# Optimization experiments

Hardware: AMD Instinct MI355X
Metric: run time of the kernel (lower is better)

The kernel has to match this reference:

```python
import jax, jax.numpy as jnp
import numpy as np

EPS = 1e-5
HEADS = 16
HEAD_DIM = 64
SIG_SCALE = HEAD_DIM ** (-0.25)
DEFAULT_BIAS = -3.0

def layernorm(x, scale, offset):
    mu = jnp.mean(x, axis=-1, keepdims=True)
    var = jnp.mean(jnp.square(x - mu), axis=-1, keepdims=True)
    return (x - mu) * jax.lax.rsqrt(var + EPS) * scale + offset

def setup_inputs() -> dict:
    key = jax.random.key(0)
    ks = jax.random.split(key, 16)
    B, Nq, Nk, D, A = 2, 2048, 2048, 1024, 1024
    s = 0.02
    return {
        "query_feats": jax.random.normal(ks[0], (B, Nq, D), jnp.float32),
        "key_feats": jax.random.normal(ks[1], (B, Nk, D), jnp.float32),
        "Wq": jax.random.normal(ks[2], (A, D), jnp.float32) * s,
        "Wk": jax.random.normal(ks[3], (A, D), jnp.float32) * s,
        "Wv": jax.random.normal(ks[4], (A, D), jnp.float32) * s,
        "Wo": jax.random.normal(ks[5], (D, A), jnp.float32) * s,
        "qn_scale": jnp.ones((HEAD_DIM,), jnp.float32),
        "qn_bias": jnp.zeros((HEAD_DIM,), jnp.float32),
        "kn_scale": jnp.ones((HEAD_DIM,), jnp.float32),
        "kn_bias": jnp.zeros((HEAD_DIM,), jnp.float32),
        "ln_q_scale": jnp.ones((D,), jnp.float32),
        "ln_q_bias": jnp.zeros((D,), jnp.float32),
        "ln_out_scale": jnp.ones((D,), jnp.float32),
        "ln_out_bias": jnp.zeros((D,), jnp.float32),
        "gamma": jnp.full((D,), 1e-5, jnp.float32),
    }

def reference(query_feats, key_feats, Wq, Wk, Wv, Wo, qn_scale, qn_bias, kn_scale, kn_bias, ln_q_scale, ln_q_bias, ln_out_scale, ln_out_bias, gamma):
    B, Nq, _ = query_feats.shape
    Nk = key_feats.shape[1]
    residual = query_feats
    xq = layernorm(query_feats, ln_q_scale, ln_q_bias)  # norm_first
    # projections (torch Linear: x @ W.T)
    q = (xq @ Wq.T).reshape(B, Nq, HEADS, HEAD_DIM).transpose(0, 2, 1, 3)
    k = (key_feats @ Wk.T).reshape(B, Nk, HEADS, HEAD_DIM).transpose(0, 2, 1, 3)
    v = (key_feats @ Wv.T).reshape(B, Nk, HEADS, HEAD_DIM).transpose(0, 2, 1, 3)
    # qk-norm over head_dim, then fixed sigmoid scale
    q = layernorm(q, qn_scale, qn_bias) * SIG_SCALE
    k = layernorm(k, kn_scale, kn_bias) * SIG_SCALE
    scores = jnp.einsum('bhqd,bhkd->bhqk', q, k) + DEFAULT_BIAS
    # hardware-optimized sigmoid: 0.5*(1+tanh(0.5*x))
    attn = 0.5 * (1.0 + jnp.tanh(0.5 * scores))
    ctx = jnp.einsum('bhqk,bhkd->bhqd', attn, v)
    ctx = ctx.transpose(0, 2, 1, 3).reshape(B, Nq, HEADS * HEAD_DIM)
    out = ctx @ Wo.T
    out = gamma * out
    out = residual + out
    out = layernorm(out, ln_out_scale, ln_out_bias)  # post_norm
    return out
```

## Files before the change

kernel.cpp:

```cpp
#include <hip/hip_runtime.h>

typedef unsigned short u16;
typedef unsigned int u32;
typedef __bf16 bf16x8 __attribute__((ext_vector_type(8)));
typedef float f32x4 __attribute__((ext_vector_type(4)));
typedef float f32x16 __attribute__((ext_vector_type(16)));
typedef u16 u16x8 __attribute__((ext_vector_type(8)));
typedef u16 u16x4 __attribute__((ext_vector_type(4)));
typedef u32 u32x2 __attribute__((ext_vector_type(2)));
typedef u32 u32x4 __attribute__((ext_vector_type(4)));

#define LN_EPS 1e-5f
#define SIG_SCALE_F 0.35355339059327379f
#define NLOG2E -1.4426950408889634f
#define BIAS_L2E 4.328085122666891f

__device__ __forceinline__ u16 f2bf(float f) {
    u32 u = __builtin_bit_cast(u32, f);
    u32 r = u + 0x7fffu + ((u >> 16) & 1u);
    return (u16)(r >> 16);
}
__device__ __forceinline__ float bf2f(u16 v) {
    return __builtin_bit_cast(float, (u32)v << 16);
}
__device__ __forceinline__ u32 pk_hi(float a, float b) {
    return __builtin_amdgcn_perm(__builtin_bit_cast(u32, b), __builtin_bit_cast(u32, a),
                                 0x07060302u);
}
__device__ __forceinline__ float fast_rcp(float x) {
    float r = __builtin_bit_cast(float, 0x7EF311C3u - __builtin_bit_cast(u32, x));
    r = r * __builtin_fmaf(-x, r, 2.0f);
    r = r * __builtin_fmaf(-x, r, 2.0f);
    return r;
}

__device__ __forceinline__ void gload16(const u16* g, u16* lds) {
    __builtin_amdgcn_global_load_lds(
        (const __attribute__((address_space(1))) u32*)g,
        (__attribute__((address_space(3))) u32*)lds, 16, 0, 0);
}

__device__ __forceinline__ void gemm_core(f32x4 acc[4][4],
                                          const u16* __restrict__ A, const u16* __restrict__ B,
                                          int Kiter, int lda, int ldb,
                                          long m0, long n0, u16* As, u16* Bs) {
    const int tid = threadIdx.x;
    const int lane = tid & 63;
    const int wave = tid >> 6;
    const int r15 = lane & 15;
    const int qd = lane >> 4;
    const int wm = (wave >> 1) * 64;
    const int wn = (wave & 1) * 64;

    const int srow = wave * 16 + (lane >> 2);
    const int c0 = (lane & 3) ^ (srow & 3);
    const u16* Ap0 = A + (m0 + srow) * lda + c0 * 8;
    const u16* Ap1 = A + (m0 + srow + 64) * lda + c0 * 8;
    const u16* Bp0 = B + (n0 + srow) * ldb + c0 * 8;
    const u16* Bp1 = B + (n0 + srow + 64) * ldb + c0 * 8;
    u16* As0 = As + wave * 512;
    u16* As1 = As + (wave + 4) * 512;
    u16* Bs0 = Bs + wave * 512;
    u16* Bs1 = Bs + (wave + 4) * 512;

    for (int kt = 0; kt < Kiter; kt += 32) {
        __syncthreads();
        gload16(Ap0 + kt, As0);
        gload16(Ap1 + kt, As1);
        gload16(Bp0 + kt, Bs0);
        gload16(Bp1 + kt, Bs1);
        __syncthreads();
        bf16x8 af[4], bfr[4];
#pragma unroll
        for (int i = 0; i < 4; i++) {
            int row = wm + i * 16 + r15;
            af[i] = *(const bf16x8*)(As + row * 32 + ((qd ^ (row & 3)) * 8));
        }
#pragma unroll
        for (int j = 0; j < 4; j++) {
            int row = wn + j * 16 + r15;
            bfr[j] = *(const bf16x8*)(Bs + row * 32 + ((qd ^ (row & 3)) * 8));
        }
#pragma unroll
        for (int i = 0; i < 4; i++)
#pragma unroll
            for (int j = 0; j < 4; j++)
                acc[i][j] = __builtin_amdgcn_mfma_f32_16x16x32_bf16(af[i], bfr[j], acc[i][j], 0, 0, 0);
    }
}

__global__ __launch_bounds__(256, 3) void gemm_qkv(const u16* __restrict__ xq, const u16* __restrict__ keyb,
                                                   const u16* __restrict__ Wqb, const u16* __restrict__ Wkb,
                                                   const u16* __restrict__ Wvb,
                                                   const float* __restrict__ qns, const float* __restrict__ qnb,
                                                   const float* __restrict__ kns, const float* __restrict__ knb,
                                                   u16* __restrict__ qln, u16* __restrict__ kln,
                                                   u16* __restrict__ vt) {
    __shared__ __attribute__((aligned(16))) u16 As[128 * 32];
    __shared__ __attribute__((aligned(16))) u16 Bs[128 * 32];
    const int z = blockIdx.z;
    const u16* A = (z == 0) ? xq : keyb;
    const u16* B = (z == 0) ? Wqb : ((z == 1) ? Wkb : Wvb);
    const long m0 = (long)blockIdx.x * 128;
    const long n0 = (long)blockIdx.y * 128;

    f32x4 acc[4][4];
#pragma unroll
    for (int i = 0; i < 4; i++)
#pragma unroll
        for (int j = 0; j < 4; j++) acc[i][j] = (f32x4){0.f, 0.f, 0.f, 0.f};

    gemm_core(acc, A, B, 1024, 1024, 1024, m0, n0, As, Bs);

    const int lane = threadIdx.x & 63;
    const int wave = threadIdx.x >> 6;
    const int r15 = lane & 15;
    const int qd = lane >> 4;
    const int wm = (wave >> 1) * 64;
    const int wn = (wave & 1) * 64;

    if (z <= 1) {
        u16* C = (z == 0) ? qln : kln;
        const float* sc_ = (z == 0) ? qns : kns;
        const float* bs_ = (z == 0) ? qnb : knb;
        const float post = (z == 0) ? SIG_SCALE_F * NLOG2E : SIG_SCALE_F;
        float scl[4], bia[4];
#pragma unroll
        for (int j = 0; j < 4; j++) {
            scl[j] = sc_[j * 16 + r15] * post;
            bia[j] = bs_[j * 16 + r15] * post;
        }
#pragma unroll
        for (int i = 0; i < 4; i++) {
#pragma unroll
            for (int rr = 0; rr < 4; rr++) {
                float a0 = acc[i][0][rr], a1 = acc[i][1][rr], a2 = acc[i][2][rr], a3 = acc[i][3][rr];
                float s1 = (a0 + a1) + (a2 + a3);
                float s2 = __builtin_fmaf(a3, a3,
                           __builtin_fmaf(a2, a2, __builtin_fmaf(a1, a1, a0 * a0)));
#pragma unroll
                for (int off = 1; off <= 8; off <<= 1) {
                    s1 += __shfl_xor(s1, off, 64);
                    s2 += __shfl_xor(s2, off, 64);
                }
                float mu = s1 * (1.0f / 64.0f);
                float var = __builtin_fmaf(-mu, mu, s2 * (1.0f / 64.0f));
                float rs = rsqrtf(var + LN_EPS);
                long row = m0 + wm + i * 16 + qd * 4 + rr;
#pragma unroll
                for (int j = 0; j < 4; j++) {
                    long col = n0 + wn + j * 16 + r15;
                    float o = __builtin_fmaf((acc[i][j][rr] - mu) * rs, scl[j], bia[j]);
                    C[row * 1024 + col] = f2bf(o);
                }
            }
        }
    } else {
#pragma unroll
        for (int i = 0; i < 4; i++)
#pragma unroll
            for (int rr = 0; rr < 4; rr++) {
                int grow = (int)(m0 + wm + i * 16 + qd * 4 + rr);
                int bb = grow >> 11;
                int kk = grow & 2047;
#pragma unroll
                for (int j = 0; j < 4; j++) {
                    int col = (int)(n0 + wn + j * 16 + r15);
                    int hh = col >> 6;
                    int dd = col & 63;
                    vt[((size_t)(bb * 16 + hh) * 64 + dd) * 2048 + kk] = f2bf(acc[i][j][rr]);
                }
            }
    }
}

__global__ __launch_bounds__(256, 4) void gemm_o(const u16* __restrict__ ctx, const u16* __restrict__ Wob,
                                                 u16* __restrict__ opre) {
    __shared__ __attribute__((aligned(16))) u16 As[128 * 32];
    __shared__ __attribute__((aligned(16))) u16 Bs[128 * 32];
    const int z = blockIdx.z;
    const int koff = z * 512;
    u16* C = opre + (size_t)z * 4194304;
    const long m0 = (long)blockIdx.x * 128;
    const long n0 = (long)blockIdx.y * 128;
    f32x4 acc[4][4];
#pragma unroll
    for (int i = 0; i < 4; i++)
#pragma unroll
        for (int j = 0; j < 4; j++) acc[i][j] = (f32x4){0.f, 0.f, 0.f, 0.f};
    gemm_core(acc, ctx + koff, Wob + koff, 512, 1024, 1024, m0, n0, As, Bs);

    const int lane = threadIdx.x & 63;
    const int wave = threadIdx.x >> 6;
    const int r15 = lane & 15;
    const int qd = lane >> 4;
    const int wm = (wave >> 1) * 64;
    const int wn = (wave & 1) * 64;
#pragma unroll
    for (int i = 0; i < 4; i++)
#pragma unroll
        for (int rr = 0; rr < 4; rr++) {
            long row = m0 + wm + i * 16 + qd * 4 + rr;
#pragma unroll
            for (int j = 0; j < 4; j++)
                C[row * 1024 + n0 + wn + j * 16 + r15] = f2bf(acc[i][j][rr]);
        }
}

__device__ __forceinline__ bf16x8 frag64(const u16* base, int row, int kidx) {
    return *(const bf16x8*)(base + row * 64 + ((kidx ^ (row & 7)) * 8));
}

__global__ __launch_bounds__(512, 4) void attn_sigmoid_v12(const u16* __restrict__ q,
                                                           const u16* __restrict__ k,
                                                           const u16* __restrict__ vt,
                                                           u16* __restrict__ ctx) {
    __shared__ __attribute__((aligned(16))) u16 Sh[8192 + 16384 + 16384];
    u16* Qs = Sh;
    u16* Ks = Sh + 8192;
    u16* Vs = Sh + 8192 + 16384;
    float* Obuf = (float*)(Sh + 8192);

    const int tid = threadIdx.x;
    const int lane = tid & 63;
    const int wave = tid >> 6;
    const int l31 = lane & 31;
    const int h = lane >> 5;
    const int qsub = wave & 3;
    const int kh = wave >> 2;
    const int hd = blockIdx.x;
    const int q0 = blockIdx.y * 128;
    const int b = blockIdx.z;
    const int bh = b * 16 + hd;

    const int lr0 = lane >> 3;
    const int lc0 = lane & 7;
    const int wsub = wave & 3;
    const int kbeg = kh * 1024;

    auto kptr = [&](int slot) { return Ks + (slot * 2 + kh) * 4096; };
    auto vptr = [&](int slot) { return (slot == 2 ? Sh : Vs + slot * 8192) + kh * 4096; };

    auto stageKV = [&](int kslot, int vslot, int kc) {
        u16* kd = kptr(kslot);
        u16* vd = vptr(vslot);
#pragma unroll
        for (int i = 0; i < 2; i++) {
            int s = wsub * 2 + i;
            int row = s * 8 + lr0;
            int c = lc0 ^ (row & 7);
            gload16(k + (size_t)(b * 2048 + kc + row) * 1024 + hd * 64 + c * 8, kd + s * 512);
            gload16(vt + (size_t)(bh * 64 + row) * 2048 + kc + c * 8, vd + s * 512);
        }
    };

    {
#pragma unroll
        for (int i = 0; i < 2; i++) {
            int s = wave * 2 + i;
            int row = s * 8 + lr0;
            int c = lc0 ^ (row & 7);
            gload16(q + (size_t)(b * 2048 + q0 + row) * 1024 + hd * 64 + c * 8, Qs + s * 512);
        }
        stageKV(0, 0, kbeg);
    }
    __syncthreads();
    bf16x8 qB[4];
#pragma unroll
    for (int dblk = 0; dblk < 4; dblk++)
        qB[dblk] = frag64(Qs, qsub * 32 + l31, dblk * 2 + h);

    f32x16 accO[2];
#pragma unroll
    for (int dt = 0; dt < 2; dt++)
#pragma unroll
        for (int r = 0; r < 16; r++) accO[dt][r] = 0.f;

    u32 pg[2][4][2];

    auto do_S_mt = [&](int kslot, int mt) -> f32x16 {
        const u16* Ksh = kptr(kslot);
        f32x16 s;
#pragma unroll
        for (int r = 0; r < 16; r++) s[r] = BIAS_L2E;
        __builtin_amdgcn_s_setprio(1);
#pragma unroll
        for (int dblk = 0; dblk < 4; dblk++) {
            bf16x8 aK = frag64(Ksh, mt * 32 + l31, dblk * 2 + h);
            s = __builtin_amdgcn_mfma_f32_32x32x16_bf16(aK, qB[dblk], s, 0, 0, 0);
        }
        __builtin_amdgcn_s_setprio(0);
        return s;
    };
    auto do_sig_mt = [&](const f32x16& s, int mt) {
#pragma unroll
        for (int g = 0; g < 4; g++) {
            float p[4];
#pragma unroll
            for (int e = 0; e < 4; e++) {
                float x = 1.0f + __builtin_amdgcn_exp2f(s[g * 4 + e]);
                p[e] = fast_rcp(x);
            }
            pg[mt][g][0] = pk_hi(p[0], p[1]);
            pg[mt][g][1] = pk_hi(p[2], p[3]);
        }
    };
    auto do_PV = [&](int vslot) {
        const u16* Vsh = vptr(vslot);
        __builtin_amdgcn_s_setprio(1);
#pragma unroll
        for (int mt = 0; mt < 2; mt++)
#pragma unroll
            for (int kblk = 0; kblk < 2; kblk++) {
                int glo = kblk * 2, ghi = kblk * 2 + 1;
                u32x2 r0 = __builtin_amdgcn_permlane32_swap(pg[mt][glo][0], pg[mt][ghi][0], false, false);
                u32x2 r1 = __builtin_amdgcn_permlane32_swap(pg[mt][glo][1], pg[mt][ghi][1], false, false);
                u32x4 fr;
                fr[0] = r0[0];
                fr[1] = r1[0];
                fr[2] = r0[1];
                fr[3] = r1[1];
                bf16x8 aP = __builtin_bit_cast(bf16x8, fr);
#pragma unroll
                for (int dt = 0; dt < 2; dt++) {
                    bf16x8 bV = frag64(Vsh, dt * 32 + l31, mt * 4 + kblk * 2 + h);
                    accO[dt] = __builtin_amdgcn_mfma_f32_32x32x16_bf16(aP, bV, accO[dt], 0, 0, 0);
                }
            }
        __builtin_amdgcn_s_setprio(0);
    };

    int vs_prev = 2, vs_cur = 0, vs_next = 1;
#pragma unroll 1
    for (int it = 0; it < 16; ++it) {
        if (it < 15) stageKV((it + 1) & 1, vs_next, kbeg + (it + 1) * 64);
        f32x16 s0 = do_S_mt(it & 1, 0);
        if (it > 0) do_PV(vs_prev);
        do_sig_mt(s0, 0);
        f32x16 s1 = do_S_mt(it & 1, 1);
        do_sig_mt(s1, 1);
        __syncthreads();
        int t = vs_prev; vs_prev = vs_cur; vs_cur = vs_next; vs_next = t;
    }
    do_PV(vs_prev);

    if (kh == 1) {
#pragma unroll
        for (int dt = 0; dt < 2; dt++)
#pragma unroll
            for (int r = 0; r < 16; r++) {
                int ql = qsub * 32 + (r & 3) + 8 * (r >> 2) + 4 * h;
                Obuf[ql * 64 + dt * 32 + l31] = accO[dt][r];
            }
    }
    __syncthreads();
    if (kh == 0) {
#pragma unroll
        for (int dt = 0; dt < 2; dt++)
#pragma unroll
            for (int r = 0; r < 16; r++) {
                int ql = qsub * 32 + (r & 3) + 8 * (r >> 2) + 4 * h;
                float s = accO[dt][r] + Obuf[ql * 64 + dt * 32 + l31];
                ctx[(size_t)(b * 2048 + q0 + ql) * 1024 + hd * 64 + dt * 32 + l31] = f2bf(s);
            }
    }
}

__global__ __launch_bounds__(256) void prep(const float* __restrict__ w0, const float* __restrict__ w1,
                                            const float* __restrict__ w2, const float* __restrict__ w3,
                                            const float* __restrict__ kf, const float* __restrict__ qf,
                                            const float* __restrict__ lnq_s, const float* __restrict__ lnq_b,
                                            u16* __restrict__ wdst, u16* __restrict__ kdst,
                                            u16* __restrict__ xq) {
    const int bx = blockIdx.x;
    const int tid = threadIdx.x;
    if (bx < 6144) {
        size_t e = ((size_t)bx * 256 + tid) * 4;
        const float* src;
        u16* dst;
        if (e < 4194304) {
            src = ((e >> 20) == 0 ? w0 : (e >> 20) == 1 ? w1 : (e >> 20) == 2 ? w2 : w3) + (e & 1048575);
            dst = wdst + e;
        } else {
            size_t off = e - 4194304;
            src = kf + off;
            dst = kdst + off;
        }
        float4 xv = *(const float4*)src;
        u16x4 o;
        o[0] = f2bf(xv.x);
        o[1] = f2bf(xv.y);
        o[2] = f2bf(xv.z);
        o[3] = f2bf(xv.w);
        *(u16x4*)dst = o;
    } else {
        __shared__ float s1buf[4], s2buf[4];
        const int row = bx - 6144;
        const size_t base = (size_t)row * 1024 + tid * 4;
        const float4 xv = *(const float4*)(qf + base);
        float s1 = xv.x + xv.y + xv.z + xv.w;
        float s2 = xv.x * xv.x + xv.y * xv.y + xv.z * xv.z + xv.w * xv.w;
        int lane = tid & 63, wave = tid >> 6;
#pragma unroll
        for (int off = 32; off > 0; off >>= 1) {
            s1 += __shfl_down(s1, off, 64);
            s2 += __shfl_down(s2, off, 64);
        }
        if (lane == 0) { s1buf[wave] = s1; s2buf[wave] = s2; }
        __syncthreads();
        s1 = s1buf[0] + s1buf[1] + s1buf[2] + s1buf[3];
        s2 = s2buf[0] + s2buf[1] + s2buf[2] + s2buf[3];
        float mu = s1 * (1.0f / 1024.0f);
        float var = s2 * (1.0f / 1024.0f) - mu * mu;
        float rs = rsqrtf(var + LN_EPS);
        const float4 scv = *(const float4*)(lnq_s + tid * 4);
        const float4 bsv = *(const float4*)(lnq_b + tid * 4);
        u16x4 o;
        o[0] = f2bf((xv.x - mu) * rs * scv.x + bsv.x);
        o[1] = f2bf((xv.y - mu) * rs * scv.y + bsv.y);
        o[2] = f2bf((xv.z - mu) * rs * scv.z + bsv.z);
        o[3] = f2bf((xv.w - mu) * rs * scv.w + bsv.w);
        *(u16x4*)(xq + base) = o;
    }
}

__global__ __launch_bounds__(256) void final_ln(const float* __restrict__ resid,
                                                const u16* __restrict__ opre,
                                                const float* __restrict__ gamma,
                                                const float* __restrict__ sc,
                                                const float* __restrict__ bs,
                                                float* __restrict__ out) {
    __shared__ float s1buf[4], s2buf[4];
    const int row = blockIdx.x;
    const int tid = threadIdx.x;
    const size_t base = (size_t)row * 1024 + tid * 4;
    float4 rv = *(const float4*)(resid + base);
    u16x4 p0 = *(const u16x4*)(opre + base);
    u16x4 p1 = *(const u16x4*)(opre + 4194304 + base);
    float4 gv = *(const float4*)(gamma + tid * 4);
    float4 xv;
    xv.x = rv.x + gv.x * (bf2f(p0[0]) + bf2f(p1[0]));
    xv.y = rv.y + gv.y * (bf2f(p0[1]) + bf2f(p1[1]));
    xv.z = rv.z + gv.z * (bf2f(p0[2]) + bf2f(p1[2]));
    xv.w = rv.w + gv.w * (bf2f(p0[3]) + bf2f(p1[3]));
    float s1 = xv.x + xv.y + xv.z + xv.w;
    float s2 = xv.x * xv.x + xv.y * xv.y + xv.z * xv.z + xv.w * xv.w;
    int lane = tid & 63, wave = tid >> 6;
#pragma unroll
    for (int off = 32; off > 0; off >>= 1) {
        s1 += __shfl_down(s1, off, 64);
        s2 += __shfl_down(s2, off, 64);
    }
    if (lane == 0) { s1buf[wave] = s1; s2buf[wave] = s2; }
    __syncthreads();
    s1 = s1buf[0] + s1buf[1] + s1buf[2] + s1buf[3];
    s2 = s2buf[0] + s2buf[1] + s2buf[2] + s2buf[3];
    float mu = s1 * (1.0f / 1024.0f);
    float var = s2 * (1.0f / 1024.0f) - mu * mu;
    float rs = rsqrtf(var + LN_EPS);
    const float4 scv = *(const float4*)(sc + tid * 4);
    const float4 bsv = *(const float4*)(bs + tid * 4);
    float4 o;
    o.x = (xv.x - mu) * rs * scv.x + bsv.x;
    o.y = (xv.y - mu) * rs * scv.y + bsv.y;
    o.z = (xv.z - mu) * rs * scv.z + bsv.z;
    o.w = (xv.w - mu) * rs * scv.w + bsv.w;
    *(float4*)(out + base) = o;
}

extern "C" void kernel_launch(void* const* d_in, const int* in_sizes, int n_in,
                              void* d_out, int out_size, void* d_ws, size_t ws_size,
                              hipStream_t stream) {
    const float* qf    = (const float*)d_in[0];
    const float* kf    = (const float*)d_in[1];
    const float* Wq    = (const float*)d_in[2];
    const float* Wk    = (const float*)d_in[3];
    const float* Wv    = (const float*)d_in[4];
    const float* Wo    = (const float*)d_in[5];
    const float* qn_s  = (const float*)d_in[6];
    const float* qn_b  = (const float*)d_in[7];
    const float* kn_s  = (const float*)d_in[8];
    const float* kn_b  = (const float*)d_in[9];
    const float* lnq_s = (const float*)d_in[10];
    const float* lnq_b = (const float*)d_in[11];
    const float* lno_s = (const float*)d_in[12];
    const float* lno_b = (const float*)d_in[13];
    const float* gamma = (const float*)d_in[14];
    float* out = (float*)d_out;

    char* ws = (char*)d_ws;
    const size_t MB = 1024 * 1024;
    u16* Wqb   = (u16*)(ws + 0 * MB);
    u16* Wkb   = (u16*)(ws + 2 * MB);
    u16* Wvb   = (u16*)(ws + 4 * MB);
    u16* Wob   = (u16*)(ws + 6 * MB);
    u16* xq    = (u16*)(ws + 8 * MB);
    u16* ctx   = (u16*)(ws + 8 * MB);
    u16* keyb  = (u16*)(ws + 16 * MB);
    u16* qln   = (u16*)(ws + 24 * MB);
    u16* kln   = (u16*)(ws + 32 * MB);
    u16* vt    = (u16*)(ws + 48 * MB);
    u16* opre  = (u16*)(ws + 24 * MB);

    prep<<<dim3(10240), 256, 0, stream>>>(Wq, Wk, Wv, Wo, kf, qf, lnq_s, lnq_b, Wqb, keyb, xq);

    gemm_qkv<<<dim3(32, 8, 3), 256, 0, stream>>>(xq, keyb, Wqb, Wkb, Wvb,
                                                 qn_s, qn_b, kn_s, kn_b, qln, kln, vt);

    attn_sigmoid_v12<<<dim3(16, 16, 2), 512, 0, stream>>>(qln, kln, vt, ctx);

    gemm_o<<<dim3(32, 8, 2), 256, 0, stream>>>(ctx, Wob, opre);
    final_ln<<<dim3(4096), 256, 0, stream>>>(qf, opre, gamma, lno_s, lno_b, out);
}
```

Measured before the change: 227.3 us.

## Load K/V fragments directly from global into registers in attention kernel

Removes the LDS staging and triple-buffered K/V pipeline from the sigmoid attention kernel. Each wave now loads its K and V^T MFMA fragments straight from global memory (relying on L2 for reuse across the 4 waves sharing a key half) and shrinks shared memory to just Q plus the reduction buffer. It also replaces the Newton-iteration reciprocal with the hardware rcp instruction. This drops barriers and LDS traffic but gives up software prefetch overlap and issues redundant global loads per wave, so load latency may be exposed.

```diff
diff --git a/kernel.cpp b/kernel.cpp
--- a/kernel.cpp
+++ b/kernel.cpp
@@ -26,12 +26,6 @@
 __device__ __forceinline__ u32 pk_hi(float a, float b) {
     return __builtin_amdgcn_perm(__builtin_bit_cast(u32, b), __builtin_bit_cast(u32, a),
                                  0x07060302u);
-}
-__device__ __forceinline__ float fast_rcp(float x) {
-    float r = __builtin_bit_cast(float, 0x7EF311C3u - __builtin_bit_cast(u32, x));
-    r = r * __builtin_fmaf(-x, r, 2.0f);
-    r = r * __builtin_fmaf(-x, r, 2.0f);
-    return r;
 }
 
 __device__ __forceinline__ void gload16(const u16* g, u16* lds) {
@@ -211,15 +205,13 @@
     return *(const bf16x8*)(base + row * 64 + ((kidx ^ (row & 7)) * 8));
 }
 
-__global__ __launch_bounds__(512, 4) void attn_sigmoid_v12(const u16* __restrict__ q,
+__global__ __launch_bounds__(512, 4) void attn_sigmoid_v13(const u16* __restrict__ q,
                                                            const u16* __restrict__ k,
                                                            const u16* __restrict__ vt,
                                                            u16* __restrict__ ctx) {
-    __shared__ __attribute__((aligned(16))) u16 Sh[8192 + 16384 + 16384];
+    __shared__ __attribute__((aligned(16))) u16 Sh[16384];
     u16* Qs = Sh;
-    u16* Ks = Sh + 8192;
-    u16* Vs = Sh + 8192 + 16384;
-    float* Obuf = (float*)(Sh + 8192);
+    float* Obuf = (float*)Sh;
 
     const int tid = threadIdx.x;
     const int lane = tid & 63;
@@ -235,24 +227,6 @@
 
     const int lr0 = lane >> 3;
     const int lc0 = lane & 7;
-    const int wsub = wave & 3;
-    const int kbeg = kh * 1024;
-
-    auto kptr = [&](int slot) { return Ks + (slot * 2 + kh) * 4096; };
-    auto vptr = [&](int slot) { return (slot == 2 ? Sh : Vs + slot * 8192) + kh * 4096; };
-
-    auto stageKV = [&](int kslot, int vslot, int kc) {
-        u16* kd = kptr(kslot);
-        u16* vd = vptr(vslot);
-#pragma unroll
-        for (int i = 0; i < 2; i++) {
-            int s = wsub * 2 + i;
-            int row = s * 8 + lr0;
-            int c = lc0 ^ (row & 7);
-            gload16(k + (size_t)(b * 2048 + kc + row) * 1024 + hd * 64 + c * 8, kd + s * 512);
-            gload16(vt + (size_t)(bh * 64 + row) * 2048 + kc + c * 8, vd + s * 512);
-        }
-    };
 
     {
 #pragma unroll
@@ -262,13 +236,13 @@
             int c = lc0 ^ (row & 7);
             gload16(q + (size_t)(b * 2048 + q0 + row) * 1024 + hd * 64 + c * 8, Qs + s * 512);
         }
-        stageKV(0, 0, kbeg);
     }
     __syncthreads();
     bf16x8 qB[4];
 #pragma unroll
     for (int dblk = 0; dblk < 4; dblk++)
         qB[dblk] = frag64(Qs, qsub * 32 + l31, dblk * 2 + h);
+    __syncthreads();
 
     f32x16 accO[2];
 #pragma unroll
@@ -277,36 +251,56 @@
         for (int r = 0; r < 16; r++) accO[dt][r] = 0.f;
 
     u32 pg[2][4][2];
-
-    auto do_S_mt = [&](int kslot, int mt) -> f32x16 {
-        const u16* Ksh = kptr(kslot);
-        f32x16 s;
-#pragma unroll
-        for (int r = 0; r < 16; r++) s[r] = BIAS_L2E;
-        __builtin_amdgcn_s_setprio(1);
-#pragma unroll
-        for (int dblk = 0; dblk < 4; dblk++) {
-            bf16x8 aK = frag64(Ksh, mt * 32 + l31, dblk * 2 + h);
-            s = __builtin_amdgcn_mfma_f32_32x32x16_bf16(aK, qB[dblk], s, 0, 0, 0);
-        }
-        __builtin_amdgcn_s_setprio(0);
-        return s;
-    };
     auto do_sig_mt = [&](const f32x16& s, int mt) {
 #pragma unroll
         for (int g = 0; g < 4; g++) {
             float p[4];
 #pragma unroll
             for (int e = 0; e < 4; e++) {
-                float x = 1.0f + __builtin_amdgcn_exp2f(s[g * 4 + e]);
-                p[e] = fast_rcp(x);
+                float u = __builtin_amdgcn_exp2f(s[g * 4 + e]);
+                p[e] = __builtin_amdgcn_rcpf(1.0f + u);
             }
             pg[mt][g][0] = pk_hi(p[0], p[1]);
             pg[mt][g][1] = pk_hi(p[2], p[3]);
         }
     };
-    auto do_PV = [&](int vslot) {
-        const u16* Vsh = vptr(vslot);
+
+    const u16* kp = k + (size_t)(b * 2048 + kh * 1024) * 1024;
+    const u16* vp = vt + (size_t)(bh * 64) * 2048 + kh * 1024;
+    const int kvoff0 = l31 * 1024 + hd * 64 + h * 8;
+    const int kvoff1 = (32 + l31) * 1024 + hd * 64 + h * 8;
+    const int vvoff0 = l31 * 2048 + h * 8;
+    const int vvoff1 = (32 + l31) * 2048 + h * 8;
+
+#pragma unroll 1
+    for (int it = 0; it < 16; ++it) {
+        bf16x8 aK0[4], aK1[4];
+#pragma unroll
+        for (int dblk = 0; dblk < 4; dblk++) {
+            aK0[dblk] = *(const bf16x8*)(kp + kvoff0 + dblk * 16);
+            aK1[dblk] = *(const bf16x8*)(kp + kvoff1 + dblk * 16);
+        }
+        f32x16 s0, s1;
+#pragma unroll
+        for (int r = 0; r < 16; r++) { s0[r] = BIAS_L2E; s1[r] = BIAS_L2E; }
+        __builtin_amdgcn_s_setprio(1);
+#pragma unroll
+        for (int dblk = 0; dblk < 4; dblk++)
+            s0 = __builtin_amdgcn_mfma_f32_32x32x16_bf16(aK0[dblk], qB[dblk], s0, 0, 0, 0);
+#pragma unroll
+        for (int dblk = 0; dblk < 4; dblk++)
+            s1 = __builtin_amdgcn_mfma_f32_32x32x16_bf16(aK1[dblk], qB[dblk], s1, 0, 0, 0);
+        __builtin_amdgcn_s_setprio(0);
+
+        do_sig_mt(s0, 0);
+        bf16x8 bV0[4], bV1[4];
+#pragma unroll
+        for (int j = 0; j < 4; j++) {
+            bV0[j] = *(const bf16x8*)(vp + vvoff0 + j * 16);
+            bV1[j] = *(const bf16x8*)(vp + vvoff1 + j * 16);
+        }
+        do_sig_mt(s1, 1);
+
         __builtin_amdgcn_s_setprio(1);
 #pragma unroll
         for (int mt = 0; mt < 2; mt++)
@@ -321,29 +315,17 @@
                 fr[2] = r0[1];
                 fr[3] = r1[1];
                 bf16x8 aP = __builtin_bit_cast(bf16x8, fr);
-#pragma unroll
-                for (int dt = 0; dt < 2; dt++) {
-                    bf16x8 bV = frag64(Vsh, dt * 32 + l31, mt * 4 + kblk * 2 + h);
-                    accO[dt] = __builtin_amdgcn_mfma_f32_32x32x16_bf16(aP, bV, accO[dt], 0, 0, 0);
-                }
+                int j = mt * 2 + kblk;
+                accO[0] = __builtin_amdgcn_mfma_f32_32x32x16_bf16(aP, bV0[j], accO[0], 0, 0, 0);
+                accO[1] = __builtin_amdgcn_mfma_f32_32x32x16_bf16(aP, bV1[j], accO[1], 0, 0, 0);
             }
         __builtin_amdgcn_s_setprio(0);
-    };
-
-    int vs_prev = 2, vs_cur = 0, vs_next = 1;
-#pragma unroll 1
-    for (int it = 0; it < 16; ++it) {
-        if (it < 15) stageKV((it + 1) & 1, vs_next, kbeg + (it + 1) * 64);
-        f32x16 s0 = do_S_mt(it & 1, 0);
-        if (it > 0) do_PV(vs_prev);
-        do_sig_mt(s0, 0);
-        f32x16 s1 = do_S_mt(it & 1, 1);
-        do_sig_mt(s1, 1);
-        __syncthreads();
-        int t = vs_prev; vs_prev = vs_cur; vs_cur = vs_next; vs_next = t;
-    }
-    do_PV(vs_prev);
-
+
+        kp += 64 * 1024;
+        vp += 64;
+    }
+
+    __syncthreads();
     if (kh == 1) {
 #pragma unroll
         for (int dt = 0; dt < 2; dt++)
@@ -507,7 +489,7 @@
     gemm_qkv<<<dim3(32, 8, 3), 256, 0, stream>>>(xq, keyb, Wqb, Wkb, Wvb,
                                                  qn_s, qn_b, kn_s, kn_b, qln, kln, vt);
 
-    attn_sigmoid_v12<<<dim3(16, 16, 2), 512, 0, stream>>>(qln, kln, vt, ctx);
+    attn_sigmoid_v13<<<dim3(16, 16, 2), 512, 0, stream>>>(qln, kln, vt, ctx);
 
     gemm_o<<<dim3(32, 8, 2), 256, 0, stream>>>(ctx, Wob, opre);
     final_ln<<<dim3(4096), 256, 0, stream>>>(qf, opre, gamma, lno_s, lno_b, out);
```

After: 313.3 us. 37.8% more time.
